# Kernel tuning notes

Measured on AMD Instinct MI355X. Metric: run time of the kernel, lower is better.

The kernel has to match this reference:

```python
import jax, jax.numpy as jnp
import numpy as np

B, T, F, H = 64, 512, 132, 1024


def setup_inputs() -> dict:
    key = jax.random.key(0)
    ks = jax.random.split(key, 16)
    k = 1.0 / np.sqrt(H)
    u = lambda kk, shape: jax.random.uniform(kk, shape, jnp.float32, -k, k)
    return {
        "real_seq": jax.random.normal(ks[0], (B, T, F), jnp.float32),
        "Wih1": u(ks[1], (4 * H, F)), "Whh1": u(ks[2], (4 * H, H)),
        "bih1": u(ks[3], (4 * H,)), "bhh1": u(ks[4], (4 * H,)),
        "Wih2": u(ks[5], (4 * H, H)), "Whh2": u(ks[6], (4 * H, H)),
        "bih2": u(ks[7], (4 * H,)), "bhh2": u(ks[8], (4 * H,)),
        "Wih3": u(ks[9], (4 * H, H)), "Whh3": u(ks[10], (4 * H, H)),
        "bih3": u(ks[11], (4 * H,)), "bhh3": u(ks[12], (4 * H,)),
        "Wd": u(ks[13], (F, H)), "bd": u(ks[14], (F,)),
        "condition_num": 5, "groundtruth_num": 5,
    }


def _cell(x, h, c, Wih, Whh, bih, bhh):
    # torch LSTMCell gate order: i, f, g, o
    gates = x @ Wih.T + h @ Whh.T + bih + bhh
    i, f, g, o = jnp.split(gates, 4, axis=-1)
    c_new = jax.nn.sigmoid(f) * c + jax.nn.sigmoid(i) * jnp.tanh(g)
    h_new = jax.nn.sigmoid(o) * jnp.tanh(c_new)
    return h_new, c_new


def reference(real_seq, Wih1, Whh1, bih1, bhh1, Wih2, Whh2, bih2, bhh2,
              Wih3, Whh3, bih3, bhh3, Wd, bd, condition_num, groundtruth_num):
    batch, seq_len, _ = real_seq.shape
    hid = Whh1.shape[1]
    out_dim = Wd.shape[0]
    # static teacher-forcing schedule (numpy, as in get_condition_lst)
    gt = np.ones((100, groundtruth_num))
    con = np.zeros((100, condition_num))
    cond = jnp.asarray(np.concatenate((gt, con), 1).reshape(-1)[:seq_len],
                       jnp.float32)

    def step(carry, xs):
        h0, h1, h2, c0, c1, c2, prev_out = carry
        frame, flag = xs
        in_frame = jnp.where(flag == 1.0, frame, prev_out)
        # NOTE: faithful to source -- lstm2 gets OLD h0, lstm3 gets OLD h1
        h0n, c0n = _cell(in_frame, h0, c0, Wih1, Whh1, bih1, bhh1)
        h1n, c1n = _cell(h0, h1, c1, Wih2, Whh2, bih2, bhh2)
        h2n, c2n = _cell(h1, h2, c2, Wih3, Whh3, bih3, bhh3)
        out = h2n @ Wd.T + bd
        return (h0n, h1n, h2n, c0n, c1n, c2n, out), out

    z = jnp.zeros((batch, hid), real_seq.dtype)
    out0 = jnp.zeros((batch, out_dim), real_seq.dtype)
    _, outs = jax.lax.scan(step, (z, z, z, z, z, z, out0),
                           (jnp.swapaxes(real_seq, 0, 1), cond))
    # outs: [T, B, F] -> concat along feature axis per timestep: [B, T*F]
    return jnp.transpose(outs, (1, 0, 2)).reshape(batch, seq_len * out_dim)
```

## Files before the change

kernel.cpp:

```cpp
#include <hip/hip_runtime.h>
#include <cstdint>


#define NBLK 256
#define NTHR 512
#define Bn 64
#define Tn 512
#define Fn 132
#define Hn 1024
#define TF (Tn * Fn)
#define SRCH 65536
#define HBUF 196608
#define XTT 10240
#define WPB 86016
#define OPW 160

typedef _Float16 h8 __attribute__((ext_vector_type(8)));
typedef float f4 __attribute__((ext_vector_type(4)));

__device__ __forceinline__ float sigf(float x) { return 1.0f / (1.0f + expf(-x)); }

__device__ __forceinline__ unsigned long long cload8(const void* p) {
    return __hip_atomic_load((unsigned long long*)p, __ATOMIC_RELAXED,
                             __HIP_MEMORY_SCOPE_AGENT);
}
__device__ __forceinline__ h8 cload16(const _Float16* p) {
    union { unsigned long long u[2]; h8 v; } c;
    c.u[0] = __hip_atomic_load((unsigned long long*)p, __ATOMIC_RELAXED,
                               __HIP_MEMORY_SCOPE_AGENT);
    c.u[1] = __hip_atomic_load((unsigned long long*)p + 1, __ATOMIC_RELAXED,
                               __HIP_MEMORY_SCOPE_AGENT);
    return c.v;
}
__device__ __forceinline__ void cstore8(void* p, unsigned long long v) {
    __hip_atomic_store((unsigned long long*)p, v, __ATOMIC_RELAXED,
                       __HIP_MEMORY_SCOPE_AGENT);
}
__device__ __forceinline__ void cstore4f(void* p, float v) {
    __hip_atomic_store((float*)p, v, __ATOMIC_RELAXED, __HIP_MEMORY_SCOPE_AGENT);
}

__device__ __forceinline__ void gsyncA(unsigned* bar, unsigned ep) {
    __syncthreads();
    if (threadIdx.x == 0) {
        unsigned* cnt = bar + ((blockIdx.x >> 5) << 5);
        unsigned old = __hip_atomic_fetch_add(cnt, 1u, __ATOMIC_RELAXED,
                                              __HIP_MEMORY_SCOPE_AGENT);
        if (old == 32u * ep - 1u) {
            unsigned d = __hip_atomic_fetch_add(bar + 256, 1u, __ATOMIC_RELAXED,
                                                __HIP_MEMORY_SCOPE_AGENT);
            if (d == 8u * ep - 1u)
                __hip_atomic_store(bar + 288, ep, __ATOMIC_RELAXED,
                                   __HIP_MEMORY_SCOPE_AGENT);
        }
        while (__hip_atomic_load(bar + 288, __ATOMIC_RELAXED,
                                 __HIP_MEMORY_SCOPE_AGENT) < ep)
            __builtin_amdgcn_s_sleep(1);
    }
    __syncthreads();
}

__device__ __forceinline__ void gsyncB(unsigned* bar2, unsigned ep2) {
    __syncthreads();
    if (threadIdx.x == 0) {
        if (blockIdx.x < Fn) {
            const unsigned g = blockIdx.x >> 5;
            const unsigned cap = (g == 4) ? 4u : 32u;
            unsigned old = __hip_atomic_fetch_add(bar2 + g * 32, 1u,
                                                  __ATOMIC_RELAXED,
                                                  __HIP_MEMORY_SCOPE_AGENT);
            if (old == cap * ep2 - 1u) {
                unsigned d = __hip_atomic_fetch_add(bar2 + 160, 1u,
                                                    __ATOMIC_RELAXED,
                                                    __HIP_MEMORY_SCOPE_AGENT);
                if (d == 5u * ep2 - 1u)
                    __hip_atomic_store(bar2 + 192, ep2, __ATOMIC_RELAXED,
                                       __HIP_MEMORY_SCOPE_AGENT);
            }
        }
        while (__hip_atomic_load(bar2 + 192, __ATOMIC_RELAXED,
                                 __HIP_MEMORY_SCOPE_AGENT) < ep2)
            __builtin_amdgcn_s_sleep(1);
    }
    __syncthreads();
}


__global__ void k_bsum(const float* bih1, const float* bhh1, const float* bih2,
                       const float* bhh2, const float* bih3, const float* bhh3,
                       float* bsum) {
    int i = blockIdx.x * 256 + threadIdx.x;
    if (i >= NBLK * 48) return;
    int bidw = i / 48, r = i % 48;
    int cell = r >> 4, n = r & 15;
    int row = (n >> 2) * Hn + bidw * 4 + (n & 3);
    const float* bi = cell == 0 ? bih1 : (cell == 1 ? bih2 : bih3);
    const float* bh = cell == 0 ? bhh1 : (cell == 1 ? bhh2 : bhh3);
    bsum[i] = bi[row] + bh[row];
}

__global__ void k_convx(const float* xseq, _Float16* xT) {
    int i = blockIdx.x * 256 + threadIdx.x;
    if (i >= Tn * XTT) return;
    int t = i / XTT, r = i % XTT;
    int k8 = r >> 9, b = (r >> 3) & 63, e = r & 7;
    int f = k8 * 8 + e;
    float v = (f < Fn) ? xseq[((size_t)b * Tn + t) * Fn + f] : 0.0f;
    xT[i] = (_Float16)v;
}

__global__ void k_convw(const float* Wih1, const float* Whh1, const float* Wih2,
                        const float* Whh2, const float* Wih3, const float* Whh3,
                        _Float16* wblob) {
    int i = blockIdx.x * 256 + threadIdx.x;
    if (i >= NBLK * WPB) return;
    int bidw = i / WPB, r = i % WPB;
    int slot = r >> 9, e = r & 511;
    int w = slot / 21, s = slot - w * 21;
    int l = e >> 3, j = e & 7;
    int kq = l >> 4, n = l & 15;
    int row = (n >> 2) * Hn + bidw * 4 + (n & 3);
    const float* M;
    int K, kt;
    if (s < 4)       { M = Whh1; K = Hn; kt = w * 4 + s; }
    else if (s < 8)  { M = Wih2; K = Hn; kt = w * 4 + s - 4; }
    else if (s < 12) { M = Whh2; K = Hn; kt = w * 4 + s - 8; }
    else if (s < 16) { M = Wih3; K = Hn; kt = w * 4 + s - 12; }
    else if (s < 20) { M = Whh3; K = Hn; kt = w * 4 + s - 16; }
    else             { M = Wih1; K = Fn; kt = w; }
    int k = kt * 32 + kq * 8 + j;
    float v = 0.0f;
    if (!(s == 20 && w >= 5) && k < K) v = M[(size_t)row * K + k];
    wblob[i] = (_Float16)v;
}

__global__ void k_misc(_Float16* hT, float* opT) {
    int i = blockIdx.x * 256 + threadIdx.x;
    if (i < HBUF) hT[i] = (_Float16)0.0f;
    else if (i < HBUF + Bn * OPW) opT[i - HBUF] = 0.0f;
}


__global__ __launch_bounds__(NTHR, 2) void lstm_mfma(
    const _Float16* __restrict__ xT, const _Float16* __restrict__ wblob,
    _Float16* __restrict__ hT, float* __restrict__ opT,
    const float* __restrict__ bsum, const float* __restrict__ Wd,
    const float* __restrict__ bd, const int* __restrict__ cnum_p,
    const int* __restrict__ gnum_p, float* __restrict__ dout,
    unsigned* __restrict__ bar) {
    __shared__ float red[8 * 12 * 68 * 4];
    __shared__ float cst[768];
    __shared__ float sbias[48];
    __shared__ unsigned long long hstage[192];

    const int tid = threadIdx.x;
    const int bid = blockIdx.x;
    const int lane = tid & 63;
    const int wid = tid >> 6;
    const int laneA0 = (lane >> 4) * 512 + (lane & 15) * 8;
    unsigned* bar2 = bar + 512;

    if (tid < 48) sbias[tid] = bsum[bid * 48 + tid];
    for (int i = tid; i < 768; i += NTHR) cst[i] = 0.0f;

    h8 wfr[21];
    {
        const _Float16* wp = wblob + (size_t)bid * WPB + (size_t)(wid * 21) * 512 + lane * 8;
#pragma unroll
        for (int s2 = 0; s2 < 21; ++s2) wfr[s2] = *(const h8*)(wp + s2 * 512);
    }
    __syncthreads();

    const int gnum = gnum_p[0];
    const int per = gnum + cnum_p[0];

    unsigned epA = 0, epB = 0;
    int tmod = 0;
    for (int t = 0; t < Tn; ++t) {
        const int flag = (tmod < gnum) ? 1 : 0;
        const int tmodn = (tmod + 1 >= per) ? 0 : (tmod + 1);
        const int rb = t % 3, wb2 = (t + 1) % 3;
        const _Float16* hr = hT + (size_t)rb * HBUF;
        _Float16* hw = hT + (size_t)wb2 * HBUF;

        f4 acc[12];
#pragma unroll
        for (int i = 0; i < 12; ++i) acc[i] = (f4){0.f, 0.f, 0.f, 0.f};

        if (wid < 5) {
            if (flag) {
                const _Float16* x0 = xT + (size_t)t * XTT + wid * 2048 + laneA0;
#pragma unroll
                for (int mt = 0; mt < 4; ++mt) {
                    h8 a = *(const h8*)(x0 + mt * 128);
                    acc[mt] = __builtin_amdgcn_mfma_f32_16x16x32_f16(a, wfr[20], acc[mt], 0, 0, 0);
                }
            } else {
                const float* op0 = opT + (size_t)(lane & 15) * OPW + wid * 32 + (lane >> 4) * 8;
#pragma unroll
                for (int mt = 0; mt < 4; ++mt) {
                    const float* q = op0 + (size_t)(mt * 16) * OPW;
                    h8 a;
#pragma unroll
                    for (int e2 = 0; e2 < 4; ++e2) {
                        union { unsigned long long u; float f[2]; } c;
                        c.u = cload8(q + 2 * e2);
                        a[2 * e2] = (_Float16)c.f[0];
                        a[2 * e2 + 1] = (_Float16)c.f[1];
                    }
                    acc[mt] = __builtin_amdgcn_mfma_f32_16x16x32_f16(a, wfr[20], acc[mt], 0, 0, 0);
                }
            }
        }
        {
            const _Float16* s0 = hr + wid * 4 * 2048 + laneA0;
#pragma unroll
            for (int i2 = 0; i2 < 4; ++i2) {
#pragma unroll
                for (int mt = 0; mt < 4; ++mt) {
                    h8 a = cload16(s0 + i2 * 2048 + mt * 128);
                    acc[mt]     = __builtin_amdgcn_mfma_f32_16x16x32_f16(a, wfr[i2],     acc[mt],     0, 0, 0);
                    acc[4 + mt] = __builtin_amdgcn_mfma_f32_16x16x32_f16(a, wfr[4 + i2], acc[4 + mt], 0, 0, 0);
                }
            }
        }
        {
            const _Float16* s1 = hr + SRCH + wid * 4 * 2048 + laneA0;
#pragma unroll
            for (int i2 = 0; i2 < 4; ++i2) {
#pragma unroll
                for (int mt = 0; mt < 4; ++mt) {
                    h8 a = cload16(s1 + i2 * 2048 + mt * 128);
                    acc[4 + mt] = __builtin_amdgcn_mfma_f32_16x16x32_f16(a, wfr[8 + i2],  acc[4 + mt], 0, 0, 0);
                    acc[8 + mt] = __builtin_amdgcn_mfma_f32_16x16x32_f16(a, wfr[12 + i2], acc[8 + mt], 0, 0, 0);
                }
            }
        }
        {
            const _Float16* s2 = hr + 2 * SRCH + wid * 4 * 2048 + laneA0;
#pragma unroll
            for (int i2 = 0; i2 < 4; ++i2) {
#pragma unroll
                for (int mt = 0; mt < 4; ++mt) {
                    h8 a = cload16(s2 + i2 * 2048 + mt * 128);
                    acc[8 + mt] = __builtin_amdgcn_mfma_f32_16x16x32_f16(a, wfr[16 + i2], acc[8 + mt], 0, 0, 0);
                }
            }
        }

        {
            float* wr = red + ((size_t)(wid * 12) * 68 + (lane >> 4) * 17 + (lane & 15)) * 4;
#pragma unroll
            for (int cc = 0; cc < 3; ++cc)
#pragma unroll
                for (int mt = 0; mt < 4; ++mt)
                    *(f4*)(wr + (cc * 4 + mt) * 68 * 4) = acc[cc * 4 + mt];
        }
        __syncthreads();
        for (int idx = tid; idx < 768; idx += NTHR) {
            const int cell = idx >> 8, jj = (idx >> 6) & 3, b = idx & 63;
            const int mt = b >> 4, mq = (b >> 2) & 3, rr = b & 3;
            float gv4[4];
#pragma unroll
            for (int gt = 0; gt < 4; ++gt) {
                const int n = gt * 4 + jj;
                float v = sbias[cell * 16 + n];
#pragma unroll
                for (int w2 = 0; w2 < 8; ++w2)
                    v += red[(((w2 * 12 + cell * 4 + mt)) * 68 + mq * 17 + n) * 4 + rr];
                gv4[gt] = v;
            }
            const float cold = cst[(cell * 4 + jj) * 64 + b];
            const float cn = sigf(gv4[1]) * cold + sigf(gv4[0]) * tanhf(gv4[2]);
            cst[(cell * 4 + jj) * 64 + b] = cn;
            const float hn = sigf(gv4[3]) * tanhf(cn);
            ((_Float16*)hstage)[(cell * 64 + b) * 4 + jj] = (_Float16)hn;
        }
        __syncthreads();
        if (tid < 192) {
            const int cell = tid >> 6, b = tid & 63;
            _Float16* dst = hw + cell * SRCH + (bid >> 1) * 512 + b * 8 + 4 * (bid & 1);
            cstore8(dst, hstage[tid]);
        }

        ++epA;
        gsyncA(bar, epA);

        if (bid < Fn) {
            const _Float16* h2 = hT + (size_t)wb2 * HBUF + 2 * SRCH;
            const int ss = tid >> 6, b = tid & 63;
            const float* wdr = Wd + (size_t)bid * Hn;
            float p = 0.0f;
#pragma unroll 4
            for (int i = 0; i < 16; ++i) {
                const int k8 = ss * 16 + i;
                h8 hv = cload16(h2 + k8 * 512 + b * 8);
                const float4 w0 = *(const float4*)(wdr + k8 * 8);
                const float4 w1 = *(const float4*)(wdr + k8 * 8 + 4);
                p = fmaf((float)hv[0], w0.x, p); p = fmaf((float)hv[1], w0.y, p);
                p = fmaf((float)hv[2], w0.z, p); p = fmaf((float)hv[3], w0.w, p);
                p = fmaf((float)hv[4], w1.x, p); p = fmaf((float)hv[5], w1.y, p);
                p = fmaf((float)hv[6], w1.z, p); p = fmaf((float)hv[7], w1.w, p);
            }
            red[ss * 64 + b] = p;
            __syncthreads();
            if (tid < 64) {
                float o = bd[bid];
#pragma unroll
                for (int u = 0; u < 8; ++u) o += red[u * 64 + tid];
                __builtin_nontemporal_store(o, &dout[(size_t)tid * TF + (size_t)t * Fn + bid]);
                cstore4f(&opT[(size_t)tid * OPW + bid], o);
            }
            __syncthreads();
        }

        const bool needbar = (t < Tn - 1) && (tmodn >= gnum);
        if (needbar) {
            ++epB;
            gsyncB(bar2, epB);
        }
        tmod = tmodn;
    }
}


extern "C" void kernel_launch(void* const* d_in, const int* in_sizes, int n_in,
                              void* d_out, int out_size, void* d_ws, size_t ws_size,
                              hipStream_t stream) {
    const float* xseq = (const float*)d_in[0];
    const float* Wih1 = (const float*)d_in[1];
    const float* Whh1 = (const float*)d_in[2];
    const float* bih1 = (const float*)d_in[3];
    const float* bhh1 = (const float*)d_in[4];
    const float* Wih2 = (const float*)d_in[5];
    const float* Whh2 = (const float*)d_in[6];
    const float* bih2 = (const float*)d_in[7];
    const float* bhh2 = (const float*)d_in[8];
    const float* Wih3 = (const float*)d_in[9];
    const float* Whh3 = (const float*)d_in[10];
    const float* bih3 = (const float*)d_in[11];
    const float* bhh3 = (const float*)d_in[12];
    const float* Wd = (const float*)d_in[13];
    const float* bd = (const float*)d_in[14];
    const int* cnum_p = (const int*)d_in[15];
    const int* gnum_p = (const int*)d_in[16];

    unsigned char* ws = (unsigned char*)d_ws;
    unsigned* bar = (unsigned*)ws;
    float* bsum = (float*)(ws + 4096);
    _Float16* xT = (_Float16*)(ws + 53248);
    _Float16* wblob = (_Float16*)(ws + 53248 + 10485760);
    _Float16* hT = (_Float16*)(ws + 53248 + 10485760 + 44040192);
    float* opT = (float*)(ws + 53248 + 10485760 + 44040192 + 1179648);

    hipMemsetAsync(bar, 0, 4096, stream);
    hipLaunchKernelGGL(k_bsum, dim3((NBLK * 48 + 255) / 256), dim3(256), 0, stream,
                       bih1, bhh1, bih2, bhh2, bih3, bhh3, bsum);
    hipLaunchKernelGGL(k_convx, dim3((Tn * XTT + 255) / 256), dim3(256), 0, stream,
                       xseq, xT);
    hipLaunchKernelGGL(k_convw, dim3((NBLK * WPB + 255) / 256), dim3(256), 0, stream,
                       Wih1, Whh1, Wih2, Whh2, Wih3, Whh3, wblob);
    hipLaunchKernelGGL(k_misc, dim3((HBUF + Bn * OPW + 255) / 256), dim3(256), 0, stream,
                       hT, opT);
    hipLaunchKernelGGL(lstm_mfma, dim3(NBLK), dim3(NTHR), 0, stream,
                       xT, wblob, hT, opT, bsum, Wd, bd, cnum_p, gnum_p,
                       (float*)d_out, bar);
}
```

Before: 8.837 ms.

## Fold dense output projection into layer-1 input weights to drop second grid barrier

When the next frame comes from the previous prediction, the layer-1 input term becomes Wih1·(Wd·h2+bd). The change precomputes Wih1·Wd as extra fp16 weight fragments and Wih1·bd as an extra bias, then feeds h2 directly into layer-1 gates in the same MFMA loop. This removes the opT feedback buffer and the second grid-wide barrier (gsyncB) per timestep. It also splits the output projection over all 256 blocks using atomic adds into a zeroed output. In exchange it adds more weight registers per wave and extra MFMAs, and the fp16-rounded fused matrix and fp32 atomic accumulation change the numerics.

```diff
diff --git a/kernel.cpp b/kernel.cpp
--- a/kernel.cpp
+++ b/kernel.cpp
@@ -12,18 +12,13 @@
 #define SRCH 65536
 #define HBUF 196608
 #define XTT 10240
-#define WPB 86016
-#define OPW 160
+#define WPB 102400
 
 typedef _Float16 h8 __attribute__((ext_vector_type(8)));
 typedef float f4 __attribute__((ext_vector_type(4)));
 
 __device__ __forceinline__ float sigf(float x) { return 1.0f / (1.0f + expf(-x)); }
 
-__device__ __forceinline__ unsigned long long cload8(const void* p) {
-    return __hip_atomic_load((unsigned long long*)p, __ATOMIC_RELAXED,
-                             __HIP_MEMORY_SCOPE_AGENT);
-}
 __device__ __forceinline__ h8 cload16(const _Float16* p) {
     union { unsigned long long u[2]; h8 v; } c;
     c.u[0] = __hip_atomic_load((unsigned long long*)p, __ATOMIC_RELAXED,
@@ -35,9 +30,6 @@
 __device__ __forceinline__ void cstore8(void* p, unsigned long long v) {
     __hip_atomic_store((unsigned long long*)p, v, __ATOMIC_RELAXED,
                        __HIP_MEMORY_SCOPE_AGENT);
-}
-__device__ __forceinline__ void cstore4f(void* p, float v) {
-    __hip_atomic_store((float*)p, v, __ATOMIC_RELAXED, __HIP_MEMORY_SCOPE_AGENT);
 }
 
 __device__ __forceinline__ void gsyncA(unsigned* bar, unsigned ep) {
@@ -60,43 +52,27 @@
     __syncthreads();
 }
 
-__device__ __forceinline__ void gsyncB(unsigned* bar2, unsigned ep2) {
-    __syncthreads();
-    if (threadIdx.x == 0) {
-        if (blockIdx.x < Fn) {
-            const unsigned g = blockIdx.x >> 5;
-            const unsigned cap = (g == 4) ? 4u : 32u;
-            unsigned old = __hip_atomic_fetch_add(bar2 + g * 32, 1u,
-                                                  __ATOMIC_RELAXED,
-                                                  __HIP_MEMORY_SCOPE_AGENT);
-            if (old == cap * ep2 - 1u) {
-                unsigned d = __hip_atomic_fetch_add(bar2 + 160, 1u,
-                                                    __ATOMIC_RELAXED,
-                                                    __HIP_MEMORY_SCOPE_AGENT);
-                if (d == 5u * ep2 - 1u)
-                    __hip_atomic_store(bar2 + 192, ep2, __ATOMIC_RELAXED,
-                                       __HIP_MEMORY_SCOPE_AGENT);
-            }
-        }
-        while (__hip_atomic_load(bar2 + 192, __ATOMIC_RELAXED,
-                                 __HIP_MEMORY_SCOPE_AGENT) < ep2)
-            __builtin_amdgcn_s_sleep(1);
-    }
-    __syncthreads();
-}
-
 
 __global__ void k_bsum(const float* bih1, const float* bhh1, const float* bih2,
                        const float* bhh2, const float* bih3, const float* bhh3,
-                       float* bsum) {
+                       const float* Wih1, const float* bd,
+                       float* bsum, float* bsum2) {
     int i = blockIdx.x * 256 + threadIdx.x;
-    if (i >= NBLK * 48) return;
-    int bidw = i / 48, r = i % 48;
-    int cell = r >> 4, n = r & 15;
-    int row = (n >> 2) * Hn + bidw * 4 + (n & 3);
-    const float* bi = cell == 0 ? bih1 : (cell == 1 ? bih2 : bih3);
-    const float* bh = cell == 0 ? bhh1 : (cell == 1 ? bhh2 : bhh3);
-    bsum[i] = bi[row] + bh[row];
+    if (i < NBLK * 48) {
+        int bidw = i / 48, r = i % 48;
+        int cell = r >> 4, n = r & 15;
+        int row = (n >> 2) * Hn + bidw * 4 + (n & 3);
+        const float* bi = cell == 0 ? bih1 : (cell == 1 ? bih2 : bih3);
+        const float* bh = cell == 0 ? bhh1 : (cell == 1 ? bhh2 : bhh3);
+        bsum[i] = bi[row] + bh[row];
+    } else if (i < NBLK * 64) {
+        int ii = i - NBLK * 48;
+        int bidw = ii / 16, n = ii % 16;
+        int row = (n >> 2) * Hn + bidw * 4 + (n & 3);
+        float s = 0.0f;
+        for (int f = 0; f < Fn; ++f) s += Wih1[(size_t)row * Fn + f] * bd[f];
+        bsum2[bidw * 16 + n] = s;
+    }
 }
 
 __global__ void k_convx(const float* xseq, _Float16* xT) {
@@ -111,46 +87,55 @@
 
 __global__ void k_convw(const float* Wih1, const float* Whh1, const float* Wih2,
                         const float* Whh2, const float* Wih3, const float* Whh3,
-                        _Float16* wblob) {
+                        const float* Wd, _Float16* wblob) {
     int i = blockIdx.x * 256 + threadIdx.x;
     if (i >= NBLK * WPB) return;
     int bidw = i / WPB, r = i % WPB;
     int slot = r >> 9, e = r & 511;
-    int w = slot / 21, s = slot - w * 21;
+    int w = slot / 25, s = slot - w * 25;
     int l = e >> 3, j = e & 7;
     int kq = l >> 4, n = l & 15;
     int row = (n >> 2) * Hn + bidw * 4 + (n & 3);
-    const float* M;
-    int K, kt;
-    if (s < 4)       { M = Whh1; K = Hn; kt = w * 4 + s; }
-    else if (s < 8)  { M = Wih2; K = Hn; kt = w * 4 + s - 4; }
-    else if (s < 12) { M = Whh2; K = Hn; kt = w * 4 + s - 8; }
-    else if (s < 16) { M = Wih3; K = Hn; kt = w * 4 + s - 12; }
-    else if (s < 20) { M = Whh3; K = Hn; kt = w * 4 + s - 16; }
-    else             { M = Wih1; K = Fn; kt = w; }
-    int k = kt * 32 + kq * 8 + j;
     float v = 0.0f;
-    if (!(s == 20 && w >= 5) && k < K) v = M[(size_t)row * K + k];
+    if (s >= 21) {
+        int kt = w * 4 + (s - 21);
+        int k = kt * 32 + kq * 8 + j;
+        float acc = 0.0f;
+        for (int f = 0; f < Fn; ++f)
+            acc += Wih1[(size_t)row * Fn + f] * Wd[(size_t)f * Hn + k];
+        v = acc;
+    } else {
+        const float* M;
+        int K, kt;
+        if (s < 4)       { M = Whh1; K = Hn; kt = w * 4 + s; }
+        else if (s < 8)  { M = Wih2; K = Hn; kt = w * 4 + s - 4; }
+        else if (s < 12) { M = Whh2; K = Hn; kt = w * 4 + s - 8; }
+        else if (s < 16) { M = Wih3; K = Hn; kt = w * 4 + s - 12; }
+        else if (s < 20) { M = Whh3; K = Hn; kt = w * 4 + s - 16; }
+        else             { M = Wih1; K = Fn; kt = w; }
+        int k = kt * 32 + kq * 8 + j;
+        if (!(s == 20 && w >= 5) && k < K) v = M[(size_t)row * K + k];
+    }
     wblob[i] = (_Float16)v;
 }
 
-__global__ void k_misc(_Float16* hT, float* opT) {
+__global__ void k_misc(_Float16* hT) {
     int i = blockIdx.x * 256 + threadIdx.x;
     if (i < HBUF) hT[i] = (_Float16)0.0f;
-    else if (i < HBUF + Bn * OPW) opT[i - HBUF] = 0.0f;
 }
 
 
 __global__ __launch_bounds__(NTHR, 2) void lstm_mfma(
     const _Float16* __restrict__ xT, const _Float16* __restrict__ wblob,
-    _Float16* __restrict__ hT, float* __restrict__ opT,
-    const float* __restrict__ bsum, const float* __restrict__ Wd,
+    _Float16* __restrict__ hT, const float* __restrict__ bsum,
+    const float* __restrict__ bsum2, const float* __restrict__ Wd,
     const float* __restrict__ bd, const int* __restrict__ cnum_p,
     const int* __restrict__ gnum_p, float* __restrict__ dout,
     unsigned* __restrict__ bar) {
     __shared__ float red[8 * 12 * 68 * 4];
     __shared__ float cst[768];
     __shared__ float sbias[48];
+    __shared__ float sbias2[16];
     __shared__ unsigned long long hstage[192];
 
     const int tid = threadIdx.x;
@@ -158,27 +143,27 @@
     const int lane = tid & 63;
     const int wid = tid >> 6;
     const int laneA0 = (lane >> 4) * 512 + (lane & 15) * 8;
-    unsigned* bar2 = bar + 512;
 
     if (tid < 48) sbias[tid] = bsum[bid * 48 + tid];
+    if (tid >= 64 && tid < 80) sbias2[tid - 64] = bsum2[bid * 16 + (tid - 64)];
     for (int i = tid; i < 768; i += NTHR) cst[i] = 0.0f;
 
-    h8 wfr[21];
+    h8 wfr[25];
     {
-        const _Float16* wp = wblob + (size_t)bid * WPB + (size_t)(wid * 21) * 512 + lane * 8;
-#pragma unroll
-        for (int s2 = 0; s2 < 21; ++s2) wfr[s2] = *(const h8*)(wp + s2 * 512);
+        const _Float16* wp = wblob + (size_t)bid * WPB + (size_t)(wid * 25) * 512 + lane * 8;
+#pragma unroll
+        for (int s2 = 0; s2 < 25; ++s2) wfr[s2] = *(const h8*)(wp + s2 * 512);
     }
     __syncthreads();
 
     const int gnum = gnum_p[0];
     const int per = gnum + cnum_p[0];
 
-    unsigned epA = 0, epB = 0;
+    unsigned epA = 0;
     int tmod = 0;
     for (int t = 0; t < Tn; ++t) {
         const int flag = (tmod < gnum) ? 1 : 0;
-        const int tmodn = (tmod + 1 >= per) ? 0 : (tmod + 1);
+        const bool fused = (!flag) && (t > 0);
         const int rb = t % 3, wb2 = (t + 1) % 3;
         const _Float16* hr = hT + (size_t)rb * HBUF;
         _Float16* hw = hT + (size_t)wb2 * HBUF;
@@ -187,29 +172,12 @@
 #pragma unroll
         for (int i = 0; i < 12; ++i) acc[i] = (f4){0.f, 0.f, 0.f, 0.f};
 
-        if (wid < 5) {
-            if (flag) {
-                const _Float16* x0 = xT + (size_t)t * XTT + wid * 2048 + laneA0;
-#pragma unroll
-                for (int mt = 0; mt < 4; ++mt) {
-                    h8 a = *(const h8*)(x0 + mt * 128);
-                    acc[mt] = __builtin_amdgcn_mfma_f32_16x16x32_f16(a, wfr[20], acc[mt], 0, 0, 0);
-                }
-            } else {
-                const float* op0 = opT + (size_t)(lane & 15) * OPW + wid * 32 + (lane >> 4) * 8;
-#pragma unroll
-                for (int mt = 0; mt < 4; ++mt) {
-                    const float* q = op0 + (size_t)(mt * 16) * OPW;
-                    h8 a;
-#pragma unroll
-                    for (int e2 = 0; e2 < 4; ++e2) {
-                        union { unsigned long long u; float f[2]; } c;
-                        c.u = cload8(q + 2 * e2);
-                        a[2 * e2] = (_Float16)c.f[0];
-                        a[2 * e2 + 1] = (_Float16)c.f[1];
-                    }
-                    acc[mt] = __builtin_amdgcn_mfma_f32_16x16x32_f16(a, wfr[20], acc[mt], 0, 0, 0);
-                }
+        if (flag && wid < 5) {
+            const _Float16* x0 = xT + (size_t)t * XTT + wid * 2048 + laneA0;
+#pragma unroll
+            for (int mt = 0; mt < 4; ++mt) {
+                h8 a = *(const h8*)(x0 + mt * 128);
+                acc[mt] = __builtin_amdgcn_mfma_f32_16x16x32_f16(a, wfr[20], acc[mt], 0, 0, 0);
             }
         }
         {
@@ -238,12 +206,24 @@
         }
         {
             const _Float16* s2 = hr + 2 * SRCH + wid * 4 * 2048 + laneA0;
-#pragma unroll
-            for (int i2 = 0; i2 < 4; ++i2) {
-#pragma unroll
-                for (int mt = 0; mt < 4; ++mt) {
-                    h8 a = cload16(s2 + i2 * 2048 + mt * 128);
-                    acc[8 + mt] = __builtin_amdgcn_mfma_f32_16x16x32_f16(a, wfr[16 + i2], acc[8 + mt], 0, 0, 0);
+            if (fused) {
+#pragma unroll
+                for (int i2 = 0; i2 < 4; ++i2) {
+#pragma unroll
+                    for (int mt = 0; mt < 4; ++mt) {
+                        h8 a = cload16(s2 + i2 * 2048 + mt * 128);
+                        acc[8 + mt] = __builtin_amdgcn_mfma_f32_16x16x32_f16(a, wfr[16 + i2], acc[8 + mt], 0, 0, 0);
+                        acc[mt]     = __builtin_amdgcn_mfma_f32_16x16x32_f16(a, wfr[21 + i2], acc[mt],     0, 0, 0);
+                    }
+                }
+            } else {
+#pragma unroll
+                for (int i2 = 0; i2 < 4; ++i2) {
+#pragma unroll
+                    for (int mt = 0; mt < 4; ++mt) {
+                        h8 a = cload16(s2 + i2 * 2048 + mt * 128);
+                        acc[8 + mt] = __builtin_amdgcn_mfma_f32_16x16x32_f16(a, wfr[16 + i2], acc[8 + mt], 0, 0, 0);
+                    }
                 }
             }
         }
@@ -257,6 +237,7 @@
                     *(f4*)(wr + (cc * 4 + mt) * 68 * 4) = acc[cc * 4 + mt];
         }
         __syncthreads();
+        const float bmul = fused ? 1.0f : 0.0f;
         for (int idx = tid; idx < 768; idx += NTHR) {
             const int cell = idx >> 8, jj = (idx >> 6) & 3, b = idx & 63;
             const int mt = b >> 4, mq = (b >> 2) & 3, rr = b & 3;
@@ -265,6 +246,7 @@
             for (int gt = 0; gt < 4; ++gt) {
                 const int n = gt * 4 + jj;
                 float v = sbias[cell * 16 + n];
+                if (cell == 0) v += bmul * sbias2[n];
 #pragma unroll
                 for (int w2 = 0; w2 < 8; ++w2)
                     v += red[(((w2 * 12 + cell * 4 + mt)) * 68 + mq * 17 + n) * 4 + rr];
@@ -286,40 +268,41 @@
         ++epA;
         gsyncA(bar, epA);
 
-        if (bid < Fn) {
+        {
             const _Float16* h2 = hT + (size_t)wb2 * HBUF + 2 * SRCH;
             const int ss = tid >> 6, b = tid & 63;
-            const float* wdr = Wd + (size_t)bid * Hn;
-            float p = 0.0f;
-#pragma unroll 4
-            for (int i = 0; i < 16; ++i) {
-                const int k8 = ss * 16 + i;
-                h8 hv = cload16(h2 + k8 * 512 + b * 8);
-                const float4 w0 = *(const float4*)(wdr + k8 * 8);
-                const float4 w1 = *(const float4*)(wdr + k8 * 8 + 4);
-                p = fmaf((float)hv[0], w0.x, p); p = fmaf((float)hv[1], w0.y, p);
-                p = fmaf((float)hv[2], w0.z, p); p = fmaf((float)hv[3], w0.w, p);
-                p = fmaf((float)hv[4], w1.x, p); p = fmaf((float)hv[5], w1.y, p);
-                p = fmaf((float)hv[6], w1.z, p); p = fmaf((float)hv[7], w1.w, p);
-            }
-            red[ss * 64 + b] = p;
-            __syncthreads();
-            if (tid < 64) {
-                float o = bd[bid];
-#pragma unroll
-                for (int u = 0; u < 8; ++u) o += red[u * 64 + tid];
-                __builtin_nontemporal_store(o, &dout[(size_t)tid * TF + (size_t)t * Fn + bid]);
-                cstore4f(&opT[(size_t)tid * OPW + bid], o);
-            }
-            __syncthreads();
-        }
-
-        const bool needbar = (t < Tn - 1) && (tmodn >= gnum);
-        if (needbar) {
-            ++epB;
-            gsyncB(bar2, epB);
-        }
-        tmod = tmodn;
+            const int nj = (bid < 8) ? 2 : 1;
+            for (int j2 = 0; j2 < nj; ++j2) {
+                int f, half;
+                if (j2 == 0) {
+                    if (bid < Fn) { f = bid; half = 0; }
+                    else          { f = bid - Fn; half = 1; }
+                } else { f = bid + (NBLK - Fn); half = 1; }
+                const float* wdr = Wd + (size_t)f * Hn;
+                float p = 0.0f;
+#pragma unroll
+                for (int i = 0; i < 8; ++i) {
+                    const int k8 = half * 64 + ss * 8 + i;
+                    h8 hv = cload16(h2 + k8 * 512 + b * 8);
+                    const float4 w0 = *(const float4*)(wdr + k8 * 8);
+                    const float4 w1 = *(const float4*)(wdr + k8 * 8 + 4);
+                    p = fmaf((float)hv[0], w0.x, p); p = fmaf((float)hv[1], w0.y, p);
+                    p = fmaf((float)hv[2], w0.z, p); p = fmaf((float)hv[3], w0.w, p);
+                    p = fmaf((float)hv[4], w1.x, p); p = fmaf((float)hv[5], w1.y, p);
+                    p = fmaf((float)hv[6], w1.z, p); p = fmaf((float)hv[7], w1.w, p);
+                }
+                red[ss * 64 + b] = p;
+                __syncthreads();
+                if (tid < 64) {
+                    float o = (half == 0) ? bd[f] : 0.0f;
+#pragma unroll
+                    for (int u = 0; u < 8; ++u) o += red[u * 64 + tid];
+                    unsafeAtomicAdd(&dout[(size_t)tid * TF + (size_t)t * Fn + f], o);
+                }
+                __syncthreads();
+            }
+        }
+        tmod = (tmod + 1 >= per) ? 0 : (tmod + 1);
     }
 }
 
@@ -348,21 +331,21 @@
     unsigned char* ws = (unsigned char*)d_ws;
     unsigned* bar = (unsigned*)ws;
     float* bsum = (float*)(ws + 4096);
-    _Float16* xT = (_Float16*)(ws + 53248);
-    _Float16* wblob = (_Float16*)(ws + 53248 + 10485760);
-    _Float16* hT = (_Float16*)(ws + 53248 + 10485760 + 44040192);
-    float* opT = (float*)(ws + 53248 + 10485760 + 44040192 + 1179648);
+    float* bsum2 = (float*)(ws + 53248);
+    _Float16* xT = (_Float16*)(ws + 102400);
+    _Float16* wblob = (_Float16*)(ws + 102400 + 10485760);
+    _Float16* hT = (_Float16*)(ws + 102400 + 10485760 + 52428800);
 
     hipMemsetAsync(bar, 0, 4096, stream);
-    hipLaunchKernelGGL(k_bsum, dim3((NBLK * 48 + 255) / 256), dim3(256), 0, stream,
-                       bih1, bhh1, bih2, bhh2, bih3, bhh3, bsum);
+    hipMemsetAsync(d_out, 0, (size_t)out_size * sizeof(float), stream);
+    hipLaunchKernelGGL(k_bsum, dim3((NBLK * 64 + 255) / 256), dim3(256), 0, stream,
+                       bih1, bhh1, bih2, bhh2, bih3, bhh3, Wih1, bd, bsum, bsum2);
     hipLaunchKernelGGL(k_convx, dim3((Tn * XTT + 255) / 256), dim3(256), 0, stream,
                        xseq, xT);
     hipLaunchKernelGGL(k_convw, dim3((NBLK * WPB + 255) / 256), dim3(256), 0, stream,
-                       Wih1, Whh1, Wih2, Whh2, Wih3, Whh3, wblob);
-    hipLaunchKernelGGL(k_misc, dim3((HBUF + Bn * OPW + 255) / 256), dim3(256), 0, stream,
-                       hT, opT);
+                       Wih1, Whh1, Wih2, Whh2, Wih3, Whh3, Wd, wblob);
+    hipLaunchKernelGGL(k_misc, dim3((HBUF + 255) / 256), dim3(256), 0, stream, hT);
     hipLaunchKernelGGL(lstm_mfma, dim3(NBLK), dim3(NTHR), 0, stream,
-                       xT, wblob, hT, opT, bsum, Wd, bd, cnum_p, gnum_p,
+                       xT, wblob, hT, bsum, bsum2, Wd, bd, cnum_p, gnum_p,
                        (float*)d_out, bar);
 }
```

Result: faster. 8.587 ms (-2.8%).
